# Kernel optimization log

Measured on AMD Instinct MI355X. Metric: run time of the kernel, lower is better.

The kernel has to match this reference:

```python
import jax, jax.numpy as jnp
import numpy as np


def _sobel_kernels(dtype):
    # kornia sobel order=1, normalized: divide by sum(|k|)=8
    gx = jnp.array([[-1., 0., 1.], [-2., 0., 2.], [-1., 0., 1.]], dtype=dtype) / 8.0
    gy = gx.T
    return jnp.stack([gx, gy])[:, None]  # (2, 1, 3, 3) OIHW


def _spatial_gradient(x):
    # x: (b, c, h, w) -> gx, gy each (b, c, h, w)
    b, c, h, w = x.shape
    xp = jnp.pad(x.reshape(b * c, 1, h, w), ((0, 0), (0, 0), (1, 1), (1, 1)), mode='edge')
    k = _sobel_kernels(x.dtype)
    out = jax.lax.conv_general_dilated(
        xp, k, window_strides=(1, 1), padding='VALID',
        dimension_numbers=('NCHW', 'OIHW', 'NCHW'))  # (b*c, 2, h, w)
    out = out.reshape(b, c, 2, h, w)
    return out[:, :, 0], out[:, :, 1]


def setup_inputs() -> dict:
    key = jax.random.key(0)
    x = jax.random.normal(key, (16, 3, 512, 512), dtype=jnp.float32)
    return {"x": x}


def reference(x):
    b, c, h, w = x.shape
    gx, gy = _spatial_gradient(x)  # (b, c, h, w) each
    if c == 3:
        mag_c = jnp.sqrt(gx * gx + gy * gy + 1e-9)  # per-channel magnitude
        # first-occurrence argmax over channels matches torch .max(dim) tie-break
        idx = jnp.argmax(mag_c, axis=1)  # (b, h, w)
        gxs = jnp.take_along_axis(gx, idx[:, None], axis=1)[:, 0]  # (b, h, w)
        gys = jnp.take_along_axis(gy, idx[:, None], axis=1)[:, 0]
    else:
        gxs, gys = gx, gy
    magnitude = jnp.sqrt(gxs * gxs + gys * gys + 1e-9)
    # clipped_div(gx, gy, 10.0)
    y_tr = jnp.where(gys == 0.0, jnp.asarray(1e-9, gys.dtype), gys)
    angle = jnp.clip(gxs / y_tr, -10.0, 10.0)
    return magnitude, angle
```

## Files before the change

kernel.cpp:

```cpp
#include <hip/hip_runtime.h>

constexpr int Hc = 512;
constexpr int Wc = 512;
constexpr int Cc = 3;
constexpr int QW = Wc / 4;


__global__ __launch_bounds__(256) void sobel_mag_angle_kernel(
    const float* __restrict__ x, float* __restrict__ out, int B) {
    int tid = blockIdx.x * 256 + threadIdx.x;
    int q = tid % QW;
    int h = (tid / QW) % Hc;
    int b = tid / (QW * Hc);
    if (b >= B) return;
    int w0 = q * 4;

    const float* xb = x + (size_t)b * Cc * Hc * Wc;

    float gxa[3][4], gya[3][4];

    bool interior = (h >= 1) && (h <= Hc - 2) && (w0 >= 4) && (w0 <= Wc - 8);
    if (interior) {
#pragma unroll
        for (int c = 0; c < Cc; ++c) {
            const float* p = xb + c * (Hc * Wc) + h * Wc + w0;
            float4 m0 = *(const float4*)(p - Wc);
            float4 m1 = *(const float4*)(p);
            float4 m2 = *(const float4*)(p + Wc);
            float l0 = p[-Wc - 1], e0 = p[-Wc + 4];
            float l1 = p[-1],      e1 = p[4];
            float l2 = p[Wc - 1],  e2 = p[Wc + 4];
            float row0[6] = {l0, m0.x, m0.y, m0.z, m0.w, e0};
            float row1[6] = {l1, m1.x, m1.y, m1.z, m1.w, e1};
            float row2[6] = {l2, m2.x, m2.y, m2.z, m2.w, e2};
#pragma unroll
            for (int i = 0; i < 4; ++i) {
                float t0 = row0[i + 2] - row0[i];
                float t1 = row1[i + 2] - row1[i];
                float t2 = row2[i + 2] - row2[i];
                gxa[c][i] = 0.125f * t0 + 0.25f * t1 + 0.125f * t2;
                float u0 = row2[i]     - row0[i];
                float u1 = row2[i + 1] - row0[i + 1];
                float u2 = row2[i + 2] - row0[i + 2];
                gya[c][i] = 0.125f * u0 + 0.25f * u1 + 0.125f * u2;
            }
        }
    } else {
#pragma unroll
        for (int c = 0; c < Cc; ++c) {
            const float* p = xb + c * (Hc * Wc);
#pragma unroll
            for (int i = 0; i < 4; ++i) {
                int w = w0 + i;
                int wm = w - 1 < 0 ? 0 : w - 1;
                int wp = w + 1 > Wc - 1 ? Wc - 1 : w + 1;
                int hm = h - 1 < 0 ? 0 : h - 1;
                int hp = h + 1 > Hc - 1 ? Hc - 1 : h + 1;
                float a00 = p[hm * Wc + wm], a01 = p[hm * Wc + w], a02 = p[hm * Wc + wp];
                float a10 = p[h * Wc + wm],                         a12 = p[h * Wc + wp];
                float a20 = p[hp * Wc + wm], a21 = p[hp * Wc + w], a22 = p[hp * Wc + wp];
                gxa[c][i] = 0.125f * (a02 - a00) + 0.25f * (a12 - a10) + 0.125f * (a22 - a20);
                gya[c][i] = 0.125f * (a20 - a00) + 0.25f * (a21 - a01) + 0.125f * (a22 - a02);
            }
        }
    }

    float mout[4], aout[4];
#pragma unroll
    for (int i = 0; i < 4; ++i) {
        float bgx = gxa[0][i], bgy = gya[0][i];
        float bm = sqrtf(bgx * bgx + bgy * bgy + 1e-9f);
#pragma unroll
        for (int c = 1; c < Cc; ++c) {
            float cgx = gxa[c][i], cgy = gya[c][i];
            float m = sqrtf(cgx * cgx + cgy * cgy + 1e-9f);
            if (m > bm) { bm = m; bgx = cgx; bgy = cgy; }
        }
        mout[i] = bm;
        float yt = (bgy == 0.0f) ? 1e-9f : bgy;
        float a = bgx / yt;
        aout[i] = fminf(fmaxf(a, -10.0f), 10.0f);
    }

    size_t obase = ((size_t)b * Hc + h) * Wc + w0;
    size_t npix = (size_t)B * Hc * Wc;
    *(float4*)(out + obase) = make_float4(mout[0], mout[1], mout[2], mout[3]);
    *(float4*)(out + npix + obase) = make_float4(aout[0], aout[1], aout[2], aout[3]);
}

extern "C" void kernel_launch(void* const* d_in, const int* in_sizes, int n_in,
                              void* d_out, int out_size, void* d_ws, size_t ws_size,
                              hipStream_t stream) {
    const float* x = (const float*)d_in[0];
    float* out = (float*)d_out;
    int B = in_sizes[0] / (Cc * Hc * Wc);
    int total_threads = B * Hc * QW;
    int blocks = (total_threads + 255) / 256;
    sobel_mag_angle_kernel<<<blocks, 256, 0, stream>>>(x, out, B);
}
```

Measured before the change: 113.0 us.

## Process eight pixels per thread with branchless clamped edges and fast math

Each thread now computes 8 output pixels instead of 4 and loads two float4s per row. Edge handling is folded into clamped row and column indices, which removes the separate scalar boundary path. The per-channel argmax is done in a running fashion, and sqrt and division are replaced with AMD hardware sqrt and reciprocal intrinsics. A launch-bounds occupancy hint is added. The approximate reciprocal can give slightly different angles, and the launch assumes the thread count divides evenly by 256.

```diff
diff --git a/kernel.cpp b/kernel.cpp
--- a/kernel.cpp
+++ b/kernel.cpp
@@ -1,91 +1,80 @@
 #include <hip/hip_runtime.h>
+
 
 constexpr int Hc = 512;
 constexpr int Wc = 512;
 constexpr int Cc = 3;
-constexpr int QW = Wc / 4;
+constexpr int PW = 8;
+constexpr int TPR = Wc / PW;
 
-
-__global__ __launch_bounds__(256) void sobel_mag_angle_kernel(
+__global__ __launch_bounds__(256, 4) void sobel_mag_angle_kernel(
     const float* __restrict__ x, float* __restrict__ out, int B) {
     int tid = blockIdx.x * 256 + threadIdx.x;
-    int q = tid % QW;
-    int h = (tid / QW) % Hc;
-    int b = tid / (QW * Hc);
-    if (b >= B) return;
-    int w0 = q * 4;
+    int lane = tid & (TPR - 1);
+    int h = (tid / TPR) & (Hc - 1);
+    int b = tid / (TPR * Hc);
+    int w0 = lane * PW;
 
     const float* xb = x + (size_t)b * Cc * Hc * Wc;
+    int hm = h > 0 ? h - 1 : 0;
+    int hp = h < Hc - 1 ? h + 1 : h;
+    int wl = w0 > 0 ? w0 - 1 : 0;
+    int wr = w0 + PW < Wc ? w0 + PW : Wc - 1;
 
-    float gxa[3][4], gya[3][4];
+    float bm[PW], bgx[PW], bgy[PW];
 
-    bool interior = (h >= 1) && (h <= Hc - 2) && (w0 >= 4) && (w0 <= Wc - 8);
-    if (interior) {
 #pragma unroll
-        for (int c = 0; c < Cc; ++c) {
-            const float* p = xb + c * (Hc * Wc) + h * Wc + w0;
-            float4 m0 = *(const float4*)(p - Wc);
-            float4 m1 = *(const float4*)(p);
-            float4 m2 = *(const float4*)(p + Wc);
-            float l0 = p[-Wc - 1], e0 = p[-Wc + 4];
-            float l1 = p[-1],      e1 = p[4];
-            float l2 = p[Wc - 1],  e2 = p[Wc + 4];
-            float row0[6] = {l0, m0.x, m0.y, m0.z, m0.w, e0};
-            float row1[6] = {l1, m1.x, m1.y, m1.z, m1.w, e1};
-            float row2[6] = {l2, m2.x, m2.y, m2.z, m2.w, e2};
+    for (int c = 0; c < Cc; ++c) {
+        const float* base = xb + c * (Hc * Wc);
+        const float* pm = base + hm * Wc;
+        const float* pc = base + h * Wc;
+        const float* pp = base + hp * Wc;
+        float4 a0 = *(const float4*)(pm + w0), a1 = *(const float4*)(pm + w0 + 4);
+        float4 b0 = *(const float4*)(pc + w0), b1 = *(const float4*)(pc + w0 + 4);
+        float4 c0 = *(const float4*)(pp + w0), c1 = *(const float4*)(pp + w0 + 4);
+        float lm = pm[wl], rm = pm[wr];
+        float lc = pc[wl], rc = pc[wr];
+        float lp = pp[wl], rp = pp[wr];
+        float r0[10] = {lm, a0.x, a0.y, a0.z, a0.w, a1.x, a1.y, a1.z, a1.w, rm};
+        float r1[10] = {lc, b0.x, b0.y, b0.z, b0.w, b1.x, b1.y, b1.z, b1.w, rc};
+        float r2[10] = {lp, c0.x, c0.y, c0.z, c0.w, c1.x, c1.y, c1.z, c1.w, rp};
 #pragma unroll
-            for (int i = 0; i < 4; ++i) {
-                float t0 = row0[i + 2] - row0[i];
-                float t1 = row1[i + 2] - row1[i];
-                float t2 = row2[i + 2] - row2[i];
-                gxa[c][i] = 0.125f * t0 + 0.25f * t1 + 0.125f * t2;
-                float u0 = row2[i]     - row0[i];
-                float u1 = row2[i + 1] - row0[i + 1];
-                float u2 = row2[i + 2] - row0[i + 2];
-                gya[c][i] = 0.125f * u0 + 0.25f * u1 + 0.125f * u2;
-            }
-        }
-    } else {
-#pragma unroll
-        for (int c = 0; c < Cc; ++c) {
-            const float* p = xb + c * (Hc * Wc);
-#pragma unroll
-            for (int i = 0; i < 4; ++i) {
-                int w = w0 + i;
-                int wm = w - 1 < 0 ? 0 : w - 1;
-                int wp = w + 1 > Wc - 1 ? Wc - 1 : w + 1;
-                int hm = h - 1 < 0 ? 0 : h - 1;
-                int hp = h + 1 > Hc - 1 ? Hc - 1 : h + 1;
-                float a00 = p[hm * Wc + wm], a01 = p[hm * Wc + w], a02 = p[hm * Wc + wp];
-                float a10 = p[h * Wc + wm],                         a12 = p[h * Wc + wp];
-                float a20 = p[hp * Wc + wm], a21 = p[hp * Wc + w], a22 = p[hp * Wc + wp];
-                gxa[c][i] = 0.125f * (a02 - a00) + 0.25f * (a12 - a10) + 0.125f * (a22 - a20);
-                gya[c][i] = 0.125f * (a20 - a00) + 0.25f * (a21 - a01) + 0.125f * (a22 - a02);
+        for (int i = 0; i < PW; ++i) {
+            float t0 = r0[i + 2] - r0[i];
+            float t1 = r1[i + 2] - r1[i];
+            float t2 = r2[i + 2] - r2[i];
+            float gx = 0.125f * (t0 + t2) + 0.25f * t1;
+            float u0 = r2[i]     - r0[i];
+            float u1 = r2[i + 1] - r0[i + 1];
+            float u2 = r2[i + 2] - r0[i + 2];
+            float gy = 0.125f * (u0 + u2) + 0.25f * u1;
+            float m = __builtin_amdgcn_sqrtf(gx * gx + gy * gy + 1e-9f);
+            if (c == 0) {
+                bm[i] = m; bgx[i] = gx; bgy[i] = gy;
+            } else {
+                bool gt = m > bm[i];
+                bm[i] = gt ? m : bm[i];
+                bgx[i] = gt ? gx : bgx[i];
+                bgy[i] = gt ? gy : bgy[i];
             }
         }
     }
 
-    float mout[4], aout[4];
+    float mo[PW], ao[PW];
 #pragma unroll
-    for (int i = 0; i < 4; ++i) {
-        float bgx = gxa[0][i], bgy = gya[0][i];
-        float bm = sqrtf(bgx * bgx + bgy * bgy + 1e-9f);
-#pragma unroll
-        for (int c = 1; c < Cc; ++c) {
-            float cgx = gxa[c][i], cgy = gya[c][i];
-            float m = sqrtf(cgx * cgx + cgy * cgy + 1e-9f);
-            if (m > bm) { bm = m; bgx = cgx; bgy = cgy; }
-        }
-        mout[i] = bm;
-        float yt = (bgy == 0.0f) ? 1e-9f : bgy;
-        float a = bgx / yt;
-        aout[i] = fminf(fmaxf(a, -10.0f), 10.0f);
+    for (int i = 0; i < PW; ++i) {
+        mo[i] = bm[i];
+        float yt = (bgy[i] == 0.0f) ? 1e-9f : bgy[i];
+        float a = bgx[i] * __builtin_amdgcn_rcpf(yt);
+        ao[i] = fminf(fmaxf(a, -10.0f), 10.0f);
     }
 
     size_t obase = ((size_t)b * Hc + h) * Wc + w0;
     size_t npix = (size_t)B * Hc * Wc;
-    *(float4*)(out + obase) = make_float4(mout[0], mout[1], mout[2], mout[3]);
-    *(float4*)(out + npix + obase) = make_float4(aout[0], aout[1], aout[2], aout[3]);
+    *(float4*)(out + obase)            = make_float4(mo[0], mo[1], mo[2], mo[3]);
+    *(float4*)(out + obase + 4)        = make_float4(mo[4], mo[5], mo[6], mo[7]);
+    *(float4*)(out + npix + obase)     = make_float4(ao[0], ao[1], ao[2], ao[3]);
+    *(float4*)(out + npix + obase + 4) = make_float4(ao[4], ao[5], ao[6], ao[7]);
 }
 
 extern "C" void kernel_launch(void* const* d_in, const int* in_sizes, int n_in,
@@ -94,7 +83,7 @@
     const float* x = (const float*)d_in[0];
     float* out = (float*)d_out;
     int B = in_sizes[0] / (Cc * Hc * Wc);
-    int total_threads = B * Hc * QW;
-    int blocks = (total_threads + 255) / 256;
+    int total_threads = B * Hc * TPR;
+    int blocks = total_threads / 256;
     sobel_mag_angle_kernel<<<blocks, 256, 0, stream>>>(x, out, B);
 }
```

Measured after the change: 106.4 us. -5.8%, faster.
